# Performance work log

Measured on AMD Instinct MI355X. Metric: run time of the kernel, lower is better.

## Reference

```python
import jax, jax.numpy as jnp
import numpy as np

B, T, N = 8, 12, 256
T_IN = S_IN = P_IN = 32
O_IN = 64
HID = 64
OUT = 64
HEADS = 4


def setup_inputs() -> dict:
    key = jax.random.key(0)
    ks = jax.random.split(key, 26)
    f = lambda k, shape: jax.random.normal(k, shape, jnp.float32) * 0.05
    return {
        'x': jax.random.normal(ks[0], (B, T, N, O_IN), jnp.float32),
        'adj': jax.random.randint(ks[1], (B, T, N, N), 0, 2, jnp.int32),
        'te': jax.random.normal(ks[2], (B, T, T_IN), jnp.float32),
        'se': jax.random.normal(ks[3], (N, S_IN), jnp.float32),
        'pe': jax.random.normal(ks[4], (N, P_IN), jnp.float32),
        # SPGAT linear layers
        'Wt': f(ks[5], (T_IN, HID)), 'bt': f(ks[6], (HID,)),
        'Ws': f(ks[7], (S_IN, HID)), 'bs': f(ks[8], (HID,)),
        'Wp': f(ks[9], (P_IN, HID)), 'bp': f(ks[10], (HID,)),
        'Wfc': f(ks[11], (HID, OUT)), 'bfc': f(ks[12], (OUT,)),
        'Wout': f(ks[13], (2 * OUT, OUT)), 'bout': f(ks[14], (OUT,)),
        # GAT layer 1 (heads=HEADS, concat)
        'W1': f(ks[15], (O_IN, HEADS * HID)), 'b1': f(ks[16], (HEADS * HID,)),
        'a1_src': f(ks[17], (HEADS, HID)), 'a1_dst': f(ks[18], (HEADS, HID)),
        # GAT layer 2 (heads=1)
        'W2': f(ks[19], (HEADS * HID, OUT)), 'b2': f(ks[20], (OUT,)),
        'a2_src': f(ks[21], (1, OUT)), 'a2_dst': f(ks[22], (1, OUT)),
    }


def _gat_conv(h, mask, W, b, a_src, a_dst, heads):
    # h: [B,T,N,Fin]; mask: [B,T,N,N] bool, mask[...,i,j] => edge i->j (coo row=src, col=dst)
    d = W.shape[1] // heads
    hp = (h @ W).reshape(h.shape[0], h.shape[1], h.shape[2], heads, d)  # [B,T,N,H,d]
    es = jnp.einsum('btnhd,hd->bthn', hp, a_src)  # source attention logits
    ed = jnp.einsum('btnhd,hd->bthn', hp, a_dst)  # target attention logits
    # scores[...,h,i,j] = leaky(es_i + ed_j), softmax over sources i per target j
    sc = jax.nn.leaky_relu(es[..., :, None] + ed[..., None, :], 0.2)  # [B,T,H,N,N]
    sc = jnp.where(mask[:, :, None, :, :], sc, jnp.float32(-1e9))
    alpha = jax.nn.softmax(sc, axis=-2)
    out = jnp.einsum('bthij,btihd->btjhd', alpha, hp)  # aggregate at target j
    return out.reshape(h.shape[0], h.shape[1], h.shape[2], heads * d) + b


def reference(x, adj, te, se, pe, Wt, bt, Ws, bs, Wp, bp, Wfc, bfc, Wout, bout,
              W1, b1, a1_src, a1_dst, W2, b2, a2_src, a2_dst):
    mask = adj != 0
    t = (te @ Wt + bt) @ Wfc + bfc          # [B,T,OUT]
    s = (se @ Ws + bs) @ Wfc + bfc          # [N,OUT]
    p = (pe @ Wp + bp) @ Wfc + bfc          # [N,OUT]
    sp = jnp.concatenate([s, p], axis=-1) @ Wout + bout  # [N,OUT]
    st = sp[None, None, :, :] + t[:, :, None, :]         # [B,T,N,OUT]
    h = jax.nn.elu(_gat_conv(x, mask, W1, b1, a1_src, a1_dst, HEADS))
    od = _gat_conv(h, mask, W2, b2, a2_src, a2_dst, 1)   # [B,T,N,OUT]
    return jnp.concatenate([od, st], axis=-1) @ Wout + bout
```

## Files before the change

kernel.cpp:

```cpp
#include <hip/hip_runtime.h>
#include <hip/hip_bf16.h>
#include <cstdint>

#define NNODE 256
#define NBT   96
#define LOG2E 1.4426950408889634f

typedef __attribute__((ext_vector_type(8))) short short8;
typedef __attribute__((ext_vector_type(4))) float f32x4;

__device__ __forceinline__ unsigned pack_bf16x2(float a, float b) {
  unsigned ua = __float_as_uint(a);
  unsigned ub = __float_as_uint(b);
  unsigned ra = (ua + 0x7FFFu + ((ua >> 16) & 1u)) >> 16;
  unsigned rb = ((ub + 0x7FFFu + ((ub >> 16) & 1u)) >> 16) << 16;
  return ra | rb;
}
__device__ __forceinline__ unsigned short bf16_rn(float a) {
  unsigned ua = __float_as_uint(a);
  return (unsigned short)((ua + 0x7FFFu + ((ua >> 16) & 1u)) >> 16);
}

__global__ __launch_bounds__(256) void setup_kernel(
    const int* __restrict__ adj, unsigned* __restrict__ mb,
    const float* __restrict__ te, const float* __restrict__ se, const float* __restrict__ pe,
    const float* __restrict__ Wt, const float* __restrict__ bt_,
    const float* __restrict__ Ws, const float* __restrict__ bs_,
    const float* __restrict__ Wp, const float* __restrict__ bp_,
    const float* __restrict__ Wfc, const float* __restrict__ bfc,
    const float* __restrict__ Wout, const float* __restrict__ bout,
    const float* __restrict__ W1, const float* __restrict__ W2,
    float* __restrict__ tW, float* __restrict__ spW,
    unsigned short* __restrict__ WoT, unsigned short* __restrict__ W1T,
    unsigned short* __restrict__ W2T) {
  const int blk = blockIdx.x, tid = threadIdx.x;
  __shared__ float A[64], Bv[64], C[64], D[64];

  if (blk < 768) {
    const int bt = blk >> 3, w = blk & 7, j = tid;
    const int* a = adj + (size_t)bt * NNODE * NNODE + (size_t)w * 32 * NNODE;
    unsigned v = 0;
#pragma unroll
    for (int b = 0; b < 32; ++b)
      v |= (a[b * NNODE + j] != 0 ? 1u : 0u) << b;
    mb[((size_t)bt * 8 + w) * 256 + j] = v;
  } else if (blk < 864) {
    const int row = blk - 768, j = tid & 63;
    if (tid < 64) {
      float h = bt_[j];
      for (int k = 0; k < 32; ++k) h += te[row * 32 + k] * Wt[k * 64 + j];
      A[j] = h;
    }
    __syncthreads();
    if (tid < 64) {
      float tv = bfc[j];
      for (int k = 0; k < 64; ++k) tv += A[k] * Wfc[k * 64 + j];
      Bv[j] = tv;
    }
    __syncthreads();
    if (tid < 64) {
      float tw = bout[j];
      for (int d = 0; d < 64; ++d) tw += Bv[d] * Wout[(64 + d) * 64 + j];
      tW[row * 64 + j] = tw;
    }
  } else if (blk < 1120) {
    const int n = blk - 864, j = tid & 63;
    float spv = 0.f;
    if (tid < 64) {
      float sh = bs_[j], ph = bp_[j];
      for (int k = 0; k < 32; ++k) {
        sh += se[n * 32 + k] * Ws[k * 64 + j];
        ph += pe[n * 32 + k] * Wp[k * 64 + j];
      }
      A[j] = sh; Bv[j] = ph;
    }
    __syncthreads();
    if (tid < 64) {
      float sv = bfc[j], pv = bfc[j];
      for (int k = 0; k < 64; ++k) {
        sv += A[k] * Wfc[k * 64 + j];
        pv += Bv[k] * Wfc[k * 64 + j];
      }
      C[j] = sv; D[j] = pv;
    }
    __syncthreads();
    if (tid < 64) {
      spv = bout[j];
      for (int k = 0; k < 64; ++k)
        spv += C[k] * Wout[k * 64 + j] + D[k] * Wout[(64 + k) * 64 + j];
    }
    __syncthreads();
    if (tid < 64) A[j] = spv;
    __syncthreads();
    if (tid < 64) {
      float spw = 0.f;
      for (int d = 0; d < 64; ++d) spw += A[d] * Wout[(64 + d) * 64 + j];
      spW[n * 64 + j] = spw;
    }
  } else if (blk == 1120) {
    {
      const int c = tid >> 2, d0 = (tid & 3) * 16;
#pragma unroll
      for (int i = 0; i < 16; ++i)
        WoT[c * 64 + d0 + i] = bf16_rn(Wout[(size_t)(d0 + i) * 64 + c]);
    }
    const int k = tid;
#pragma unroll
    for (int d = 0; d < 64; ++d)
      W2T[d * 256 + k] = bf16_rn(W2[(size_t)k * 64 + d]);
  } else {
    const int hd = tid;
    unsigned u[32];
#pragma unroll
    for (int p = 0; p < 32; ++p) {
      float a = W1[(size_t)(2 * p) * 256 + hd];
      float b = W1[(size_t)(2 * p + 1) * 256 + hd];
      u[p] = pack_bf16x2(a, b);
    }
    unsigned* o = (unsigned*)(W1T + (size_t)hd * 64);
#pragma unroll
    for (int p = 0; p < 8; ++p) {
      uint4 v;
      v.x = u[4 * p + 0]; v.y = u[4 * p + 1];
      v.z = u[4 * p + 2]; v.w = u[4 * p + 3];
      *reinterpret_cast<uint4*>(o + 4 * p) = v;
    }
  }
}

__global__ __launch_bounds__(512, 2) void fused1_kernel(
    const float* __restrict__ x, const unsigned* __restrict__ W1Tu,
    const unsigned* __restrict__ mbg, const float* __restrict__ a1s,
    const float* __restrict__ a1d, const float* __restrict__ b1,
    unsigned* __restrict__ hgl) {
  const int bt = blockIdx.x, head = blockIdx.y, z = blockIdx.z, tid = threadIdx.x;
  __shared__ union U {
    unsigned xb[256][36];
    unsigned hpT[64][132];
    unsigned short ob[128][72];
  } sm;
  __shared__ unsigned w1t[64][36];
  __shared__ unsigned mbs[1024];
  __shared__ float ess[256], eds[128], asv[64], adv[64];

  if (tid < 256) {
    const float* xrow = x + ((size_t)bt * NNODE + tid) * 64;
    unsigned u[32];
#pragma unroll
    for (int p = 0; p < 16; ++p) {
      float4 v = reinterpret_cast<const float4*>(xrow)[p];
      u[2 * p] = pack_bf16x2(v.x, v.y);
      u[2 * p + 1] = pack_bf16x2(v.z, v.w);
    }
#pragma unroll
    for (int p = 0; p < 8; ++p) {
      uint4 v; v.x = u[4 * p]; v.y = u[4 * p + 1]; v.z = u[4 * p + 2]; v.w = u[4 * p + 3];
      *reinterpret_cast<uint4*>(&sm.xb[tid][4 * p]) = v;
    }
    const int w = tid >> 5, col = (tid & 31) * 4;
    *reinterpret_cast<uint4*>(&mbs[w * 128 + col]) =
        *reinterpret_cast<const uint4*>(&mbg[(size_t)bt * 2048 + w * 256 + z * 128 + col]);
  } else {
    const int tt = tid - 256;
#pragma unroll
    for (int c = 0; c < 2; ++c) {
      const int idx = tt * 2 + c;
      const int r = idx >> 3, c4 = (idx & 7) * 4;
      *reinterpret_cast<uint4*>(&w1t[r][c4]) =
          *reinterpret_cast<const uint4*>(&W1Tu[(size_t)(head * 64 + r) * 32 + c4]);
    }
    if (tt < 64) asv[tt] = a1s[head * 64 + tt];
    else if (tt < 128) adv[tt - 64] = a1d[head * 64 + (tt - 64)];
  }
  __syncthreads();

  const int lane = tid & 63, wv = tid >> 6;
  const int m = lane & 15, q = lane >> 4;
  const f32x4 z4 = {0.f, 0.f, 0.f, 0.f};

  f32x4 cf[4][2];
#pragma unroll
  for (int mt = 0; mt < 4; ++mt)
#pragma unroll
    for (int nt = 0; nt < 2; ++nt) cf[mt][nt] = z4;
#pragma unroll
  for (int kt = 0; kt < 2; ++kt) {
    short8 af[4], bf[2];
#pragma unroll
    for (int mt = 0; mt < 4; ++mt)
      af[mt] = *reinterpret_cast<const short8*>(&w1t[mt * 16 + m][kt * 16 + q * 4]);
#pragma unroll
    for (int nt = 0; nt < 2; ++nt)
      bf[nt] = *reinterpret_cast<const short8*>(&sm.xb[wv * 32 + nt * 16 + m][kt * 16 + q * 4]);
#pragma unroll
    for (int mt = 0; mt < 4; ++mt)
#pragma unroll
      for (int nt = 0; nt < 2; ++nt)
        cf[mt][nt] = __builtin_amdgcn_mfma_f32_16x16x32_bf16(af[mt], bf[nt], cf[mt][nt], 0, 0, 0);
  }
  __syncthreads();

  {
    unsigned short* hpT16 = reinterpret_cast<unsigned short*>(&sm.hpT[0][0]);
#pragma unroll
    for (int mt = 0; mt < 4; ++mt)
#pragma unroll
      for (int nt = 0; nt < 2; ++nt)
#pragma unroll
        for (int reg = 0; reg < 4; ++reg) {
          const int d = mt * 16 + q * 4 + reg;
          const int n = wv * 32 + nt * 16 + m;
          hpT16[d * 264 + n] = bf16_rn(cf[mt][nt][reg]);
        }
  }
  __syncthreads();

  if (tid < 256) {
    const int n = tid;
    const unsigned sh = (n & 1) * 16;
    float s = 0.f;
#pragma unroll 8
    for (int d = 0; d < 64; ++d) {
      unsigned u = sm.hpT[d][n >> 1];
      s += __uint_as_float((u >> sh) << 16) * asv[d];
    }
    ess[n] = s * LOG2E;
  } else if (tid < 384) {
    const int jl = tid - 256;
    const int n = z * 128 + jl;
    const unsigned sh = (n & 1) * 16;
    float s = 0.f;
#pragma unroll 8
    for (int d = 0; d < 64; ++d) {
      unsigned u = sm.hpT[d][n >> 1];
      s += __uint_as_float((u >> sh) << 16) * adv[d];
    }
    eds[jl] = s * LOG2E;
  }
  __syncthreads();

  f32x4 cacc[4], cden = z4;
#pragma unroll
  for (int nt = 0; nt < 4; ++nt) cacc[nt] = z4;
  const float edv = eds[wv * 16 + m];
  const short8 ones8 = {(short)0x3F80, (short)0x3F80, (short)0x3F80, (short)0x3F80,
                        (short)0x3F80, (short)0x3F80, (short)0x3F80, (short)0x3F80};

  for (int kt = 0; kt < 8; ++kt) {
    short8 bfr[4];
#pragma unroll
    for (int nt = 0; nt < 4; ++nt)
      bfr[nt] = *reinterpret_cast<const short8*>(&sm.hpT[nt * 16 + m][kt * 16 + q * 4]);
    float e[8];
    *reinterpret_cast<float4*>(&e[0]) = *reinterpret_cast<const float4*>(&ess[kt * 32 + q * 8]);
    *reinterpret_cast<float4*>(&e[4]) = *reinterpret_cast<const float4*>(&ess[kt * 32 + q * 8 + 4]);
    const unsigned bits = mbs[kt * 128 + wv * 16 + m] >> (q * 8);
    float pv[8];
#pragma unroll
    for (int r = 0; r < 8; ++r) {
      float sc = e[r] + edv;
      sc = fmaxf(sc, 0.2f * sc);
      pv[r] = ((bits >> r) & 1u) ? exp2f(sc) : 0.f;
    }
    union { unsigned u[4]; short8 s; } A;
#pragma unroll
    for (int h = 0; h < 4; ++h) A.u[h] = pack_bf16x2(pv[2 * h], pv[2 * h + 1]);
#pragma unroll
    for (int nt = 0; nt < 4; ++nt)
      cacc[nt] = __builtin_amdgcn_mfma_f32_16x16x32_bf16(A.s, bfr[nt], cacc[nt], 0, 0, 0);
    cden = __builtin_amdgcn_mfma_f32_16x16x32_bf16(A.s, ones8, cden, 0, 0, 0);
  }
  __syncthreads();

  float b1v[4];
#pragma unroll
  for (int nt = 0; nt < 4; ++nt) b1v[nt] = b1[head * 64 + nt * 16 + m];
#pragma unroll
  for (int reg = 0; reg < 4; ++reg) {
    const int jl = wv * 16 + q * 4 + reg;
    const float inv = 1.f / fmaxf(cden[reg], 1e-30f);
#pragma unroll
    for (int nt = 0; nt < 4; ++nt) {
      float v = cacc[nt][reg] * inv + b1v[nt];
      v = v > 0.f ? v : expm1f(v);
      sm.ob[jl][nt * 16 + m] = bf16_rn(v);
    }
  }
  __syncthreads();

  unsigned* go = hgl + (size_t)bt * 32768 + (size_t)z * 128 * 128 + head * 32;
#pragma unroll
  for (int c = 0; c < 2; ++c) {
    const int idx = tid * 2 + c;
    const int jl = idx >> 3, c4 = (idx & 7) * 4;
    *reinterpret_cast<uint4*>(&go[(size_t)jl * 128 + c4]) =
        *reinterpret_cast<const uint4*>(&sm.ob[jl][c4 * 2]);
  }
}

__global__ __launch_bounds__(512, 2) void fused2_kernel(
    const unsigned* __restrict__ hglu, const unsigned* __restrict__ W2Tu,
    const unsigned* __restrict__ mbg, const float* __restrict__ a2s,
    const float* __restrict__ a2d, const float* __restrict__ b2,
    const unsigned* __restrict__ WoTu, const float* __restrict__ spW,
    const float* __restrict__ tW, float* __restrict__ out) {
  const int bt = blockIdx.x, jh = blockIdx.y, tid = threadIdx.x;
  const int jbase = jh * 128;
  __shared__ union U {
    struct { unsigned h_c[256][36]; unsigned w2t_c[64][36]; } fs;
    unsigned hpT[64][132];
    unsigned short ob[128][72];
  } sm;
  __shared__ unsigned wol[64][36];
  __shared__ unsigned mbs[1024];
  __shared__ float ess[256], eds[128];
  __shared__ float a2sv[64], a2dv[64];

  {
    int row = tid >> 3, col = (tid & 7) * 4;
    *reinterpret_cast<uint4*>(&wol[row][col]) =
        *reinterpret_cast<const uint4*>(&WoTu[row * 32 + col]);
  }
  if (tid < 256) {
    int w = tid >> 5, col = (tid & 31) * 4;
    *reinterpret_cast<uint4*>(&mbs[w * 128 + col]) =
        *reinterpret_cast<const uint4*>(&mbg[(size_t)bt * 2048 + w * 256 + jbase + col]);
  }
  if (tid >= 384 && tid < 448) a2sv[tid - 384] = a2s[tid - 384];
  else if (tid >= 448) a2dv[tid - 448] = a2d[tid - 448];

  const int lane = tid & 63, wv = tid >> 6;
  const int m = lane & 15, q = lane >> 4;
  const f32x4 z4 = {0.f, 0.f, 0.f, 0.f};

  f32x4 cf[4][2];
#pragma unroll
  for (int mt = 0; mt < 4; ++mt)
#pragma unroll
    for (int nt = 0; nt < 2; ++nt) cf[mt][nt] = z4;

  for (int kc = 0; kc < 4; ++kc) {
    __syncthreads();
#pragma unroll
    for (int c = 0; c < 4; ++c) {
      int i4 = tid + c * 512;
      int n = i4 >> 3, col = (i4 & 7) * 4;
      *reinterpret_cast<uint4*>(&sm.fs.h_c[n][col]) =
          *reinterpret_cast<const uint4*>(&hglu[(size_t)bt * 32768 + n * 128 + kc * 32 + col]);
    }
    {
      int d = tid >> 3, col = (tid & 7) * 4;
      *reinterpret_cast<uint4*>(&sm.fs.w2t_c[d][col]) =
          *reinterpret_cast<const uint4*>(&W2Tu[d * 128 + kc * 32 + col]);
    }
    __syncthreads();
#pragma unroll
    for (int kt2 = 0; kt2 < 2; ++kt2) {
      short8 af[4], bf[2];
#pragma unroll
      for (int mt = 0; mt < 4; ++mt)
        af[mt] = *reinterpret_cast<const short8*>(&sm.fs.w2t_c[mt * 16 + m][kt2 * 16 + q * 4]);
#pragma unroll
      for (int nt = 0; nt < 2; ++nt)
        bf[nt] = *reinterpret_cast<const short8*>(&sm.fs.h_c[wv * 32 + nt * 16 + m][kt2 * 16 + q * 4]);
#pragma unroll
      for (int mt = 0; mt < 4; ++mt)
#pragma unroll
        for (int nt = 0; nt < 2; ++nt)
          cf[mt][nt] = __builtin_amdgcn_mfma_f32_16x16x32_bf16(af[mt], bf[nt], cf[mt][nt], 0, 0, 0);
    }
  }
  __syncthreads();

  {
    unsigned short* hpT16 = reinterpret_cast<unsigned short*>(&sm.hpT[0][0]);
#pragma unroll
    for (int mt = 0; mt < 4; ++mt)
#pragma unroll
      for (int nt = 0; nt < 2; ++nt)
#pragma unroll
        for (int reg = 0; reg < 4; ++reg) {
          const int d = mt * 16 + q * 4 + reg;
          const int n = wv * 32 + nt * 16 + m;
          hpT16[d * 264 + n] = bf16_rn(cf[mt][nt][reg]);
        }
  }
  __syncthreads();

  if (tid < 256) {
    const int n = tid;
    const unsigned sh = (n & 1) * 16;
    float s = 0.f;
#pragma unroll 8
    for (int d = 0; d < 64; ++d) {
      unsigned u = sm.hpT[d][n >> 1];
      s += __uint_as_float((u >> sh) << 16) * a2sv[d];
    }
    ess[n] = s * LOG2E;
  } else if (tid < 384) {
    const int jl = tid - 256;
    const int n = jbase + jl;
    const unsigned sh = (n & 1) * 16;
    float s = 0.f;
#pragma unroll 8
    for (int d = 0; d < 64; ++d) {
      unsigned u = sm.hpT[d][n >> 1];
      s += __uint_as_float((u >> sh) << 16) * a2dv[d];
    }
    eds[jl] = s * LOG2E;
  }
  __syncthreads();

  f32x4 cacc[4], cden = z4;
#pragma unroll
  for (int nt = 0; nt < 4; ++nt) cacc[nt] = z4;
  const float edv = eds[wv * 16 + m];
  const short8 ones8 = {(short)0x3F80, (short)0x3F80, (short)0x3F80, (short)0x3F80,
                        (short)0x3F80, (short)0x3F80, (short)0x3F80, (short)0x3F80};

  for (int kt = 0; kt < 8; ++kt) {
    short8 bfr[4];
#pragma unroll
    for (int nt = 0; nt < 4; ++nt)
      bfr[nt] = *reinterpret_cast<const short8*>(&sm.hpT[nt * 16 + m][kt * 16 + q * 4]);
    float e[8];
    *reinterpret_cast<float4*>(&e[0]) = *reinterpret_cast<const float4*>(&ess[kt * 32 + q * 8]);
    *reinterpret_cast<float4*>(&e[4]) = *reinterpret_cast<const float4*>(&ess[kt * 32 + q * 8 + 4]);
    const unsigned bits = mbs[kt * 128 + wv * 16 + m] >> (q * 8);
    float pv[8];
#pragma unroll
    for (int r = 0; r < 8; ++r) {
      float sc = e[r] + edv;
      sc = fmaxf(sc, 0.2f * sc);
      pv[r] = ((bits >> r) & 1u) ? exp2f(sc) : 0.f;
    }
    union { unsigned u[4]; short8 s; } A;
#pragma unroll
    for (int h = 0; h < 4; ++h) A.u[h] = pack_bf16x2(pv[2 * h], pv[2 * h + 1]);
#pragma unroll
    for (int nt = 0; nt < 4; ++nt)
      cacc[nt] = __builtin_amdgcn_mfma_f32_16x16x32_bf16(A.s, bfr[nt], cacc[nt], 0, 0, 0);
    cden = __builtin_amdgcn_mfma_f32_16x16x32_bf16(A.s, ones8, cden, 0, 0, 0);
  }
  __syncthreads();

  float b2v[4];
#pragma unroll
  for (int nt = 0; nt < 4; ++nt) b2v[nt] = b2[nt * 16 + m];
#pragma unroll
  for (int reg = 0; reg < 4; ++reg) {
    const int jl = wv * 16 + q * 4 + reg;
    const float inv = 1.f / fmaxf(cden[reg], 1e-30f);
#pragma unroll
    for (int nt = 0; nt < 4; ++nt)
      sm.ob[jl][nt * 16 + m] = bf16_rn(cacc[nt][reg] * inv + b2v[nt]);
  }
  __syncthreads();

  f32x4 c2[4];
#pragma unroll
  for (int ct = 0; ct < 4; ++ct) c2[ct] = z4;
#pragma unroll
  for (int kt2 = 0; kt2 < 2; ++kt2) {
    short8 a2f = *reinterpret_cast<const short8*>(&sm.ob[wv * 16 + m][kt2 * 32 + q * 8]);
#pragma unroll
    for (int ct = 0; ct < 4; ++ct) {
      short8 bw = *reinterpret_cast<const short8*>(&wol[ct * 16 + m][kt2 * 16 + q * 4]);
      c2[ct] = __builtin_amdgcn_mfma_f32_16x16x32_bf16(a2f, bw, c2[ct], 0, 0, 0);
    }
  }
  float tWv[4];
#pragma unroll
  for (int ct = 0; ct < 4; ++ct) tWv[ct] = tW[bt * 64 + ct * 16 + m];
#pragma unroll
  for (int reg = 0; reg < 4; ++reg) {
    const int j = jbase + wv * 16 + q * 4 + reg;
#pragma unroll
    for (int ct = 0; ct < 4; ++ct) {
      const int cc = ct * 16 + m;
      out[((size_t)bt * NNODE + j) * 64 + cc] =
          c2[ct][reg] + spW[j * 64 + cc] + tWv[ct];
    }
  }
}

extern "C" void kernel_launch(void* const* d_in, const int* in_sizes, int n_in,
                              void* d_out, int out_size, void* d_ws, size_t ws_size,
                              hipStream_t stream) {
  const float* x    = (const float*)d_in[0];
  const int*   adj  = (const int*)d_in[1];
  const float* te   = (const float*)d_in[2];
  const float* se   = (const float*)d_in[3];
  const float* pe   = (const float*)d_in[4];
  const float* Wt   = (const float*)d_in[5];
  const float* bt_  = (const float*)d_in[6];
  const float* Ws   = (const float*)d_in[7];
  const float* bs_  = (const float*)d_in[8];
  const float* Wp   = (const float*)d_in[9];
  const float* bp_  = (const float*)d_in[10];
  const float* Wfc  = (const float*)d_in[11];
  const float* bfc  = (const float*)d_in[12];
  const float* Wout = (const float*)d_in[13];
  const float* bout = (const float*)d_in[14];
  const float* W1   = (const float*)d_in[15];
  const float* b1   = (const float*)d_in[16];
  const float* a1s  = (const float*)d_in[17];
  const float* a1d  = (const float*)d_in[18];
  const float* W2   = (const float*)d_in[19];
  const float* b2   = (const float*)d_in[20];
  const float* a2s  = (const float*)d_in[21];
  const float* a2d  = (const float*)d_in[22];

  char* ws = (char*)d_ws;
  unsigned*       mb   = (unsigned*)(ws);
  float*          tW   = (float*)(ws + 786432);
  float*          spW  = (float*)(ws + 811008);
  unsigned short* WoT  = (unsigned short*)(ws + 876544);
  unsigned short* W1T  = (unsigned short*)(ws + 884736);
  unsigned short* W2T  = (unsigned short*)(ws + 917504);
  unsigned*       hgl  = (unsigned*)(ws + 13533184);

  setup_kernel<<<1122, 256, 0, stream>>>(adj, mb, te, se, pe, Wt, bt_, Ws, bs_,
                                         Wp, bp_, Wfc, bfc, Wout, bout, W1, W2,
                                         tW, spW, WoT, W1T, W2T);
  fused1_kernel<<<dim3(NBT, 4, 2), 512, 0, stream>>>(x, (const unsigned*)W1T, mb,
                                                     a1s, a1d, b1, hgl);
  fused2_kernel<<<dim3(NBT, 2), 512, 0, stream>>>(hgl, (const unsigned*)W2T, mb,
                                                  a2s, a2d, b2, (const unsigned*)WoT,
                                                  spW, tW, (float*)d_out);
}
```

Measured before the change: 169.8 us.

## Compute attention logits from MFMA registers and split fused2 into quarter blocks

```diff
diff --git a/kernel.cpp b/kernel.cpp
--- a/kernel.cpp
+++ b/kernel.cpp
@@ -201,6 +201,30 @@
   __syncthreads();
 
   {
+    float pes0 = 0.f, pes1 = 0.f, ped0 = 0.f, ped1 = 0.f;
+#pragma unroll
+    for (int mt = 0; mt < 4; ++mt)
+#pragma unroll
+      for (int reg = 0; reg < 4; ++reg) {
+        const int d = mt * 16 + q * 4 + reg;
+        const float a = asv[d], bdv = adv[d];
+        pes0 += cf[mt][0][reg] * a;  ped0 += cf[mt][0][reg] * bdv;
+        pes1 += cf[mt][1][reg] * a;  ped1 += cf[mt][1][reg] * bdv;
+      }
+    pes0 += __shfl_xor(pes0, 16, 64); pes0 += __shfl_xor(pes0, 32, 64);
+    pes1 += __shfl_xor(pes1, 16, 64); pes1 += __shfl_xor(pes1, 32, 64);
+    ped0 += __shfl_xor(ped0, 16, 64); ped0 += __shfl_xor(ped0, 32, 64);
+    ped1 += __shfl_xor(ped1, 16, 64); ped1 += __shfl_xor(ped1, 32, 64);
+    if (q == 0) {
+      const int n0 = wv * 32 + m, n1 = wv * 32 + 16 + m;
+      ess[n0] = pes0 * LOG2E;
+      ess[n1] = pes1 * LOG2E;
+      if ((n0 >> 7) == z) eds[n0 & 127] = ped0 * LOG2E;
+      if ((n1 >> 7) == z) eds[n1 & 127] = ped1 * LOG2E;
+    }
+  }
+
+  {
     unsigned short* hpT16 = reinterpret_cast<unsigned short*>(&sm.hpT[0][0]);
 #pragma unroll
     for (int mt = 0; mt < 4; ++mt)
@@ -212,30 +236,6 @@
           const int n = wv * 32 + nt * 16 + m;
           hpT16[d * 264 + n] = bf16_rn(cf[mt][nt][reg]);
         }
-  }
-  __syncthreads();
-
-  if (tid < 256) {
-    const int n = tid;
-    const unsigned sh = (n & 1) * 16;
-    float s = 0.f;
-#pragma unroll 8
-    for (int d = 0; d < 64; ++d) {
-      unsigned u = sm.hpT[d][n >> 1];
-      s += __uint_as_float((u >> sh) << 16) * asv[d];
-    }
-    ess[n] = s * LOG2E;
-  } else if (tid < 384) {
-    const int jl = tid - 256;
-    const int n = z * 128 + jl;
-    const unsigned sh = (n & 1) * 16;
-    float s = 0.f;
-#pragma unroll 8
-    for (int d = 0; d < 64; ++d) {
-      unsigned u = sm.hpT[d][n >> 1];
-      s += __uint_as_float((u >> sh) << 16) * adv[d];
-    }
-    eds[jl] = s * LOG2E;
   }
   __syncthreads();
 
@@ -298,116 +298,127 @@
   }
 }
 
-__global__ __launch_bounds__(512, 2) void fused2_kernel(
+__global__ __launch_bounds__(256, 2) void fused2_kernel(
     const unsigned* __restrict__ hglu, const unsigned* __restrict__ W2Tu,
     const unsigned* __restrict__ mbg, const float* __restrict__ a2s,
     const float* __restrict__ a2d, const float* __restrict__ b2,
     const unsigned* __restrict__ WoTu, const float* __restrict__ spW,
     const float* __restrict__ tW, float* __restrict__ out) {
   const int bt = blockIdx.x, jh = blockIdx.y, tid = threadIdx.x;
-  const int jbase = jh * 128;
+  const int jbase = jh * 64;
   __shared__ union U {
     struct { unsigned h_c[256][36]; unsigned w2t_c[64][36]; } fs;
     unsigned hpT[64][132];
-    unsigned short ob[128][72];
+    unsigned short ob[64][72];
   } sm;
   __shared__ unsigned wol[64][36];
-  __shared__ unsigned mbs[1024];
-  __shared__ float ess[256], eds[128];
+  __shared__ unsigned mbs[512];
+  __shared__ float ess[256], eds[64];
   __shared__ float a2sv[64], a2dv[64];
 
-  {
-    int row = tid >> 3, col = (tid & 7) * 4;
+#pragma unroll
+  for (int c = 0; c < 2; ++c) {
+    int idx = tid * 2 + c;
+    int row = idx >> 3, col = (idx & 7) * 4;
     *reinterpret_cast<uint4*>(&wol[row][col]) =
         *reinterpret_cast<const uint4*>(&WoTu[row * 32 + col]);
   }
-  if (tid < 256) {
-    int w = tid >> 5, col = (tid & 31) * 4;
-    *reinterpret_cast<uint4*>(&mbs[w * 128 + col]) =
+  if (tid < 128) {
+    int w = tid >> 4, col = (tid & 15) * 4;
+    *reinterpret_cast<uint4*>(&mbs[w * 64 + col]) =
         *reinterpret_cast<const uint4*>(&mbg[(size_t)bt * 2048 + w * 256 + jbase + col]);
-  }
-  if (tid >= 384 && tid < 448) a2sv[tid - 384] = a2s[tid - 384];
-  else if (tid >= 448) a2dv[tid - 448] = a2d[tid - 448];
+  } else if (tid < 192) {
+    a2sv[tid - 128] = a2s[tid - 128];
+  } else {
+    a2dv[tid - 192] = a2d[tid - 192];
+  }
 
   const int lane = tid & 63, wv = tid >> 6;
   const int m = lane & 15, q = lane >> 4;
   const f32x4 z4 = {0.f, 0.f, 0.f, 0.f};
 
-  f32x4 cf[4][2];
+  f32x4 cf[4][4];
 #pragma unroll
   for (int mt = 0; mt < 4; ++mt)
 #pragma unroll
-    for (int nt = 0; nt < 2; ++nt) cf[mt][nt] = z4;
+    for (int nt = 0; nt < 4; ++nt) cf[mt][nt] = z4;
 
   for (int kc = 0; kc < 4; ++kc) {
     __syncthreads();
 #pragma unroll
-    for (int c = 0; c < 4; ++c) {
-      int i4 = tid + c * 512;
+    for (int c = 0; c < 8; ++c) {
+      int i4 = tid + c * 256;
       int n = i4 >> 3, col = (i4 & 7) * 4;
       *reinterpret_cast<uint4*>(&sm.fs.h_c[n][col]) =
           *reinterpret_cast<const uint4*>(&hglu[(size_t)bt * 32768 + n * 128 + kc * 32 + col]);
     }
-    {
-      int d = tid >> 3, col = (tid & 7) * 4;
+#pragma unroll
+    for (int c = 0; c < 2; ++c) {
+      int idx = tid * 2 + c;
+      int d = idx >> 3, col = (idx & 7) * 4;
       *reinterpret_cast<uint4*>(&sm.fs.w2t_c[d][col]) =
           *reinterpret_cast<const uint4*>(&W2Tu[d * 128 + kc * 32 + col]);
     }
     __syncthreads();
 #pragma unroll
     for (int kt2 = 0; kt2 < 2; ++kt2) {
-      short8 af[4], bf[2];
+      short8 af[4], bf[4];
 #pragma unroll
       for (int mt = 0; mt < 4; ++mt)
         af[mt] = *reinterpret_cast<const short8*>(&sm.fs.w2t_c[mt * 16 + m][kt2 * 16 + q * 4]);
 #pragma unroll
-      for (int nt = 0; nt < 2; ++nt)
-        bf[nt] = *reinterpret_cast<const short8*>(&sm.fs.h_c[wv * 32 + nt * 16 + m][kt2 * 16 + q * 4]);
+      for (int nt = 0; nt < 4; ++nt)
+        bf[nt] = *reinterpret_cast<const short8*>(&sm.fs.h_c[wv * 64 + nt * 16 + m][kt2 * 16 + q * 4]);
 #pragma unroll
       for (int mt = 0; mt < 4; ++mt)
 #pragma unroll
-        for (int nt = 0; nt < 2; ++nt)
+        for (int nt = 0; nt < 4; ++nt)
           cf[mt][nt] = __builtin_amdgcn_mfma_f32_16x16x32_bf16(af[mt], bf[nt], cf[mt][nt], 0, 0, 0);
     }
   }
   __syncthreads();
+
+  {
+    float pes[4] = {0.f, 0.f, 0.f, 0.f}, ped[4] = {0.f, 0.f, 0.f, 0.f};
+#pragma unroll
+    for (int mt = 0; mt < 4; ++mt)
+#pragma unroll
+      for (int reg = 0; reg < 4; ++reg) {
+        const int d = mt * 16 + q * 4 + reg;
+        const float a = a2sv[d], bdv = a2dv[d];
+#pragma unroll
+        for (int nt = 0; nt < 4; ++nt) {
+          pes[nt] += cf[mt][nt][reg] * a;
+          ped[nt] += cf[mt][nt][reg] * bdv;
+        }
+      }
+#pragma unroll
+    for (int nt = 0; nt < 4; ++nt) {
+      pes[nt] += __shfl_xor(pes[nt], 16, 64); pes[nt] += __shfl_xor(pes[nt], 32, 64);
+      ped[nt] += __shfl_xor(ped[nt], 16, 64); ped[nt] += __shfl_xor(ped[nt], 32, 64);
+    }
+    if (q == 0) {
+#pragma unroll
+      for (int nt = 0; nt < 4; ++nt) {
+        const int n = wv * 64 + nt * 16 + m;
+        ess[n] = pes[nt] * LOG2E;
+        if (n >= jbase && n < jbase + 64) eds[n - jbase] = ped[nt] * LOG2E;
+      }
+    }
+  }
 
   {
     unsigned short* hpT16 = reinterpret_cast<unsigned short*>(&sm.hpT[0][0]);
 #pragma unroll
     for (int mt = 0; mt < 4; ++mt)
 #pragma unroll
-      for (int nt = 0; nt < 2; ++nt)
+      for (int nt = 0; nt < 4; ++nt)
 #pragma unroll
         for (int reg = 0; reg < 4; ++reg) {
           const int d = mt * 16 + q * 4 + reg;
-          const int n = wv * 32 + nt * 16 + m;
+          const int n = wv * 64 + nt * 16 + m;
           hpT16[d * 264 + n] = bf16_rn(cf[mt][nt][reg]);
         }
-  }
-  __syncthreads();
-
-  if (tid < 256) {
-    const int n = tid;
-    const unsigned sh = (n & 1) * 16;
-    float s = 0.f;
-#pragma unroll 8
-    for (int d = 0; d < 64; ++d) {
-      unsigned u = sm.hpT[d][n >> 1];
-      s += __uint_as_float((u >> sh) << 16) * a2sv[d];
-    }
-    ess[n] = s * LOG2E;
-  } else if (tid < 384) {
-    const int jl = tid - 256;
-    const int n = jbase + jl;
-    const unsigned sh = (n & 1) * 16;
-    float s = 0.f;
-#pragma unroll 8
-    for (int d = 0; d < 64; ++d) {
-      unsigned u = sm.hpT[d][n >> 1];
-      s += __uint_as_float((u >> sh) << 16) * a2dv[d];
-    }
-    eds[jl] = s * LOG2E;
   }
   __syncthreads();
 
@@ -426,7 +437,7 @@
     float e[8];
     *reinterpret_cast<float4*>(&e[0]) = *reinterpret_cast<const float4*>(&ess[kt * 32 + q * 8]);
     *reinterpret_cast<float4*>(&e[4]) = *reinterpret_cast<const float4*>(&ess[kt * 32 + q * 8 + 4]);
-    const unsigned bits = mbs[kt * 128 + wv * 16 + m] >> (q * 8);
+    const unsigned bits = mbs[kt * 64 + wv * 16 + m] >> (q * 8);
     float pv[8];
 #pragma unroll
     for (int r = 0; r < 8; ++r) {
@@ -525,7 +536,7 @@
                                          tW, spW, WoT, W1T, W2T);
   fused1_kernel<<<dim3(NBT, 4, 2), 512, 0, stream>>>(x, (const unsigned*)W1T, mb,
                                                      a1s, a1d, b1, hgl);
-  fused2_kernel<<<dim3(NBT, 2), 512, 0, stream>>>(hgl, (const unsigned*)W2T, mb,
+  fused2_kernel<<<dim3(NBT, 4), 256, 0, stream>>>(hgl, (const unsigned*)W2T, mb,
                                                   a2s, a2d, b2, (const unsigned*)WoT,
                                                   spW, tW, (float*)d_out);
 }
```

Result: no change. 168.5 us (-0.8%).
